# Optimization experiments

Hardware: AMD Instinct MI355X
Metric: run time of the kernel (lower is better)

## Reference

```python
import math
import jax, jax.numpy as jnp
import numpy as np

NUM_TOKENS = 8192
MODEL_DIM = 1024
NUM_EXPERTS = 64
CAPACITY_FACTOR = 1.0
MIN_CAPACITY = 8
SHIFT_PRIORITY = 0.5
LOAD_BALANCE_W = 0.01


def setup_inputs() -> dict:
    key = jax.random.key(0)
    k1, k2 = jax.random.split(key)
    x = jax.random.normal(k1, (NUM_TOKENS, MODEL_DIM), dtype=jnp.float32)
    # torch.nn.Linear(model_dim, num_experts, bias=False).weight -> [E, D]
    wg_weight = jax.random.normal(k2, (NUM_EXPERTS, MODEL_DIM), dtype=jnp.float32) * 0.02
    return {"x": x, "wg_weight": wg_weight}


def reference(x, wg_weight):
    S = x.shape[0]
    E = wg_weight.shape[0]
    # gate projection (fp32, as in DeepSpeed gating)
    logits = jnp.einsum('sd,ed->se', x, wg_weight)  # [S, E]
    gates = jax.nn.softmax(logits, axis=1)
    original_gates = gates

    # _capacity: ceil(S/E * capacity_factor), clamped to min_capacity (static)
    capacity = max(int(math.ceil(S / E * CAPACITY_FACTOR)), MIN_CAPACITY)

    indices1_s = jnp.argmax(gates, axis=1)                      # [S]
    mask1 = jax.nn.one_hot(indices1_s, E, dtype=jnp.int32)      # [S, E]
    exp_counts = jnp.sum(mask1, axis=0)                         # [E]

    # AuxLoss: GShard load-balance loss, zloss/entropy weights are 0
    me = jnp.mean(gates, axis=0)
    ce = jnp.mean(mask1.astype(gates.dtype), axis=0)
    l_aux = jnp.sum(me * ce) * E * LOAD_BALANCE_W

    # shifted-priority routing: sort tokens by -max_gate, roll, positional cumsum
    importance_scores = -jnp.max(gates, axis=1)                 # [S]
    sort_indices = jnp.argsort(importance_scores)               # [S]
    shift_num = int(S * SHIFT_PRIORITY)                         # static
    sort_indices = jnp.roll(sort_indices, shift_num)
    recover_indices = jnp.argsort(sort_indices)
    sorted_mask1 = mask1[sort_indices]                          # [S, E]
    sorted_cumsum1 = (jnp.cumsum(sorted_mask1, axis=0) - 1) * sorted_mask1
    locations1 = sorted_cumsum1[recover_indices]                # [S, E]

    # capacity dropping
    mask1 = mask1 * (locations1 < capacity).astype(jnp.int32)
    locations1_s = jnp.sum(locations1 * mask1, axis=1)          # [S]

    gates_masked = original_gates * mask1.astype(gates.dtype)   # [S, E]
    locations1_sc = jax.nn.one_hot(locations1_s, capacity, dtype=gates.dtype)  # [S, C]
    combine_weights = jnp.einsum('se,sc->sec', gates_masked, locations1_sc)    # [S, E, C]
    dispatch_mask = combine_weights.astype(bool)

    unrouted_token_rate = 1.0 - jnp.mean(jnp.any(dispatch_mask, axis=(-1, -2)).astype(jnp.float32))
    return l_aux, combine_weights, dispatch_mask, exp_counts, unrouted_token_rate
```

## Files before the change

### kernel.cpp

```cpp
#include <hip/hip_runtime.h>
#include <stdint.h>

#define S_TOK   8192
#define MODEL_D 1024
#define N_EXP   64
#define CAP     128
#define SHIFT   4096
#define SLAB    (N_EXP * CAP)
#define CDSIZE  ((size_t)S_TOK * SLAB)


#define OFF_EXPERT   0
#define OFF_GATE     32768
#define OFF_KEY      65536
#define OFF_KEY2     98304
#define OFF_LOC      131072
#define OFF_MEPART   163840
#define OFF_HIST     229376
#define OFF_DROP     294912
#define OFF_WGT      295936

__device__ __forceinline__ unsigned f2key(float f) {
    unsigned b = __float_as_uint(f);
    return (b & 0x80000000u) ? ~b : (b | 0x80000000u);
}

__global__ __launch_bounds__(256) void k0_transpose(const float* __restrict__ wg,
                                                    float* __restrict__ wgT) {
    int id0 = blockIdx.x * 256 + threadIdx.x;
#pragma unroll
    for (int i = 0; i < 4; ++i) {
        int id = id0 + i * 16384;
        int e = id >> 10;
        int d = id & 1023;
        wgT[d * 64 + e] = wg[id];
    }
}

__global__ __launch_bounds__(256) void k1_gemm_softmax(
    const float* __restrict__ x, const float* __restrict__ wgT,
    int* __restrict__ expert_id, float* __restrict__ gate1,
    unsigned* __restrict__ keys, float* __restrict__ me_part,
    int* __restrict__ hist_part)
{
    __shared__ float lg[32][65];
    __shared__ float mrow[32], zrow[32];
    __shared__ int   exrow[32];
    __shared__ int   hist[64];
    __shared__ float mep[4][64];

    const int tid  = threadIdx.x;
    const int lane = tid & 63;
    const int wave = __builtin_amdgcn_readfirstlane(tid >> 6);
    const int tokBase = blockIdx.x * 32 + wave * 8;

    float acc[8] = {0.f,0.f,0.f,0.f,0.f,0.f,0.f,0.f};
    const float* xrow = x + (size_t)tokBase * MODEL_D;

    for (int d = 0; d < MODEL_D; d += 4) {
        float w0 = wgT[(d + 0) * 64 + lane];
        float w1 = wgT[(d + 1) * 64 + lane];
        float w2 = wgT[(d + 2) * 64 + lane];
        float w3 = wgT[(d + 3) * 64 + lane];
#pragma unroll
        for (int t = 0; t < 8; ++t) {
            const float* xr = xrow + t * MODEL_D + d;
            acc[t] = fmaf(xr[0], w0, acc[t]);
            acc[t] = fmaf(xr[1], w1, acc[t]);
            acc[t] = fmaf(xr[2], w2, acc[t]);
            acc[t] = fmaf(xr[3], w3, acc[t]);
        }
    }
#pragma unroll
    for (int t = 0; t < 8; ++t) lg[wave * 8 + t][lane] = acc[t];
    __syncthreads();

    if (tid < 64) hist[tid] = 0;
    if (tid < 32) {
        const int t = tid;
        float m = lg[t][0]; int am = 0;
        for (int e = 1; e < 64; ++e) {
            float v = lg[t][e];
            if (v > m) { m = v; am = e; }
        }
        float z = 0.f;
        for (int e = 0; e < 64; ++e) z += expf(lg[t][e] - m);
        float rz = 1.0f / z;
        mrow[t] = m; zrow[t] = rz; exrow[t] = am;
        int sG = blockIdx.x * 32 + t;
        expert_id[sG] = am;
        gate1[sG] = rz;
        keys[sG] = f2key(-rz);
    }
    __syncthreads();

    if (tid < 32) atomicAdd(&hist[exrow[tid]], 1);
    {
        const int e = tid & 63, tg = tid >> 6;
        float p = 0.f;
        for (int t = tg; t < 32; t += 4) p += expf(lg[t][e] - mrow[t]) * zrow[t];
        mep[tg][e] = p;
    }
    __syncthreads();

    if (tid < 64) {
        me_part[blockIdx.x * 64 + tid] = mep[0][tid] + mep[1][tid] + mep[2][tid] + mep[3][tid];
        hist_part[blockIdx.x * 64 + tid] = hist[tid];
    }
}

__global__ __launch_bounds__(256) void k2_rank(const unsigned* __restrict__ keys,
                                               const int* __restrict__ expert_id,
                                               unsigned* __restrict__ key2)
{
    __shared__ uint4 k4[2048];
    const int tid = threadIdx.x;
    const uint4* kg = (const uint4*)keys;
    for (int i = tid; i < 2048; i += 256) k4[i] = kg[i];
    __syncthreads();

    const int sl = tid >> 3, part = tid & 7;
    const int sG = blockIdx.x * 32 + sl;
    const unsigned myk = ((const unsigned*)k4)[sG];
    int cnt = 0;
    const int qbase = part * 256;
    for (int q = 0; q < 256; ++q) {
        uint4 v = k4[qbase + q];
        int j = (qbase + q) * 4;
        cnt += (v.x < myk) || (v.x == myk && (j + 0) < sG);
        cnt += (v.y < myk) || (v.y == myk && (j + 1) < sG);
        cnt += (v.z < myk) || (v.z == myk && (j + 2) < sG);
        cnt += (v.w < myk) || (v.w == myk && (j + 3) < sG);
    }
    cnt += __shfl_down(cnt, 4);
    cnt += __shfl_down(cnt, 2);
    cnt += __shfl_down(cnt, 1);
    if (part == 0) {
        int pos = (cnt + SHIFT) & (S_TOK - 1);
        key2[sG] = ((unsigned)expert_id[sG] << 13) | (unsigned)pos;
    }
}

__global__ __launch_bounds__(256) void k3_loc(const unsigned* __restrict__ key2,
                                              int* __restrict__ loc,
                                              int* __restrict__ drop_part)
{
    __shared__ uint4 k4[2048];
    __shared__ int dropc;
    const int tid = threadIdx.x;
    if (tid == 0) dropc = 0;
    const uint4* kg = (const uint4*)key2;
    for (int i = tid; i < 2048; i += 256) k4[i] = kg[i];
    __syncthreads();

    const int sl = tid >> 3, part = tid & 7;
    const int sG = blockIdx.x * 32 + sl;
    const unsigned myk = ((const unsigned*)k4)[sG];
    const unsigned lo = myk & ~8191u;
    int cnt = 0;
    const int qbase = part * 256;
    for (int q = 0; q < 256; ++q) {
        uint4 v = k4[qbase + q];
        cnt += (v.x >= lo) && (v.x < myk);
        cnt += (v.y >= lo) && (v.y < myk);
        cnt += (v.z >= lo) && (v.z < myk);
        cnt += (v.w >= lo) && (v.w < myk);
    }
    cnt += __shfl_down(cnt, 4);
    cnt += __shfl_down(cnt, 2);
    cnt += __shfl_down(cnt, 1);
    if (part == 0) {
        loc[sG] = cnt;
        if (cnt >= CAP) atomicAdd(&dropc, 1);
    }
    __syncthreads();
    if (tid == 0) drop_part[blockIdx.x] = dropc;
}

__global__ __launch_bounds__(256) void k4_write(const int* __restrict__ expert_id,
                                                const float* __restrict__ gate1,
                                                const int* __restrict__ loc,
                                                const float* __restrict__ me_part,
                                                const int* __restrict__ hist_part,
                                                const int* __restrict__ drop_part,
                                                float* __restrict__ out)
{
    const int b = blockIdx.x;
    if (b < S_TOK) {
        const int es = expert_id[b];
        const int lc = loc[b];
        const float g = gate1[b];
        const bool kept = (lc < CAP);
        const int hot = es * CAP + lc;
        float* outC = out + 1 + (size_t)b * SLAB;
        float* outD = outC + CDSIZE;
        for (int i = threadIdx.x; i < SLAB; i += 256) {
            bool is = kept && (i == hot);
            outC[i] = is ? g : 0.0f;
            outD[i] = is ? 1.0f : 0.0f;
        }
    } else {
        __shared__ float contrib[64];
        const int tid = threadIdx.x;
        if (tid < 64) {
            float ms = 0.f; int hs = 0;
            for (int p = 0; p < 256; ++p) {
                ms += me_part[p * 64 + tid];
                hs += hist_part[p * 64 + tid];
            }
            out[1 + 2 * CDSIZE + tid] = (float)hs;
            contrib[tid] = (ms * (1.0f / S_TOK)) * ((float)hs * (1.0f / S_TOK));
        }
        __syncthreads();
        if (tid == 0) {
            float sum = 0.f;
            for (int e = 0; e < 64; ++e) sum += contrib[e];
            out[0] = sum * (float)N_EXP * 0.01f;
            int dr = 0;
            for (int p = 0; p < 256; ++p) dr += drop_part[p];
            out[1 + 2 * CDSIZE + 64] = (float)dr * (1.0f / S_TOK);
        }
    }
}

extern "C" void kernel_launch(void* const* d_in, const int* in_sizes, int n_in,
                              void* d_out, int out_size, void* d_ws, size_t ws_size,
                              hipStream_t stream) {
    (void)in_sizes; (void)n_in; (void)out_size; (void)ws_size;
    const float* x  = (const float*)d_in[0];
    const float* wg = (const float*)d_in[1];
    float* out = (float*)d_out;
    char* ws = (char*)d_ws;

    int*      expert_id = (int*)(ws + OFF_EXPERT);
    float*    gate1     = (float*)(ws + OFF_GATE);
    unsigned* keys      = (unsigned*)(ws + OFF_KEY);
    unsigned* key2      = (unsigned*)(ws + OFF_KEY2);
    int*      loc       = (int*)(ws + OFF_LOC);
    float*    me_part   = (float*)(ws + OFF_MEPART);
    int*      hist_part = (int*)(ws + OFF_HIST);
    int*      drop_part = (int*)(ws + OFF_DROP);
    float*    wgT       = (float*)(ws + OFF_WGT);

    hipLaunchKernelGGL(k0_transpose,    dim3(64),   dim3(256), 0, stream, wg, wgT);
    hipLaunchKernelGGL(k1_gemm_softmax, dim3(256),  dim3(256), 0, stream, x, wgT,
                       expert_id, gate1, keys, me_part, hist_part);
    hipLaunchKernelGGL(k2_rank,         dim3(256),  dim3(256), 0, stream, keys, expert_id, key2);
    hipLaunchKernelGGL(k3_loc,          dim3(256),  dim3(256), 0, stream, key2, loc, drop_part);
    hipLaunchKernelGGL(k4_write,        dim3(8193), dim3(256), 0, stream,
                       expert_id, gate1, loc, me_part, hist_part, drop_part, out);
}
```

Measured before the change: 753.2 us.

## Zero-fill output with vector stores and scatter hot entries; stage x in LDS

The per-token slab writer is replaced by a grid-stride float4 zero fill of the whole output. The location kernel then scatters only the single nonzero combine and dispatch entry per kept token, and the load-balance reduction moves into a small one-block final kernel. The gate GEMM now stages x chunks in shared memory and reads a float4-repacked weight layout. The rank loops rotate their start index per part, which is meant to reduce LDS bank conflicts. The cost is an extra ordering dependency: the fill must finish before the scatter writes.

```diff
diff --git a/kernel.cpp b/kernel.cpp
--- a/kernel.cpp
+++ b/kernel.cpp
@@ -8,13 +8,13 @@
 #define SHIFT   4096
 #define SLAB    (N_EXP * CAP)
 #define CDSIZE  ((size_t)S_TOK * SLAB)
+#define OUT_FILL4 33554448
 
 
 #define OFF_EXPERT   0
 #define OFF_GATE     32768
 #define OFF_KEY      65536
 #define OFF_KEY2     98304
-#define OFF_LOC      131072
 #define OFF_MEPART   163840
 #define OFF_HIST     229376
 #define OFF_DROP     294912
@@ -25,24 +25,32 @@
     return (b & 0x80000000u) ? ~b : (b | 0x80000000u);
 }
 
-__global__ __launch_bounds__(256) void k0_transpose(const float* __restrict__ wg,
-                                                    float* __restrict__ wgT) {
+__global__ __launch_bounds__(256) void k_fill(float4* __restrict__ out4) {
+    const float4 z = make_float4(0.f, 0.f, 0.f, 0.f);
+    size_t i = (size_t)blockIdx.x * 256 + threadIdx.x;
+    const size_t stride = (size_t)gridDim.x * 256;
+    for (; i < OUT_FILL4; i += stride) out4[i] = z;
+}
+
+__global__ __launch_bounds__(256) void k0_repack(const float* __restrict__ wg,
+                                                 float* __restrict__ wgT4) {
     int id0 = blockIdx.x * 256 + threadIdx.x;
 #pragma unroll
     for (int i = 0; i < 4; ++i) {
         int id = id0 + i * 16384;
         int e = id >> 10;
         int d = id & 1023;
-        wgT[d * 64 + e] = wg[id];
+        wgT4[((d >> 2) * 64 + e) * 4 + (d & 3)] = wg[id];
     }
 }
 
 __global__ __launch_bounds__(256) void k1_gemm_softmax(
-    const float* __restrict__ x, const float* __restrict__ wgT,
+    const float* __restrict__ x, const float* __restrict__ wgT4,
     int* __restrict__ expert_id, float* __restrict__ gate1,
     unsigned* __restrict__ keys, float* __restrict__ me_part,
     int* __restrict__ hist_part)
 {
+    __shared__ float xs[32][256];
     __shared__ float lg[32][65];
     __shared__ float mrow[32], zrow[32];
     __shared__ int   exrow[32];
@@ -51,28 +59,41 @@
 
     const int tid  = threadIdx.x;
     const int lane = tid & 63;
-    const int wave = __builtin_amdgcn_readfirstlane(tid >> 6);
-    const int tokBase = blockIdx.x * 32 + wave * 8;
+    const int wv   = tid >> 6;
+    const int tok0 = blockIdx.x * 32;
+
+    const float4* xg  = (const float4*)x;
+    const float4* wg4 = (const float4*)wgT4;
 
     float acc[8] = {0.f,0.f,0.f,0.f,0.f,0.f,0.f,0.f};
-    const float* xrow = x + (size_t)tokBase * MODEL_D;
-
-    for (int d = 0; d < MODEL_D; d += 4) {
-        float w0 = wgT[(d + 0) * 64 + lane];
-        float w1 = wgT[(d + 1) * 64 + lane];
-        float w2 = wgT[(d + 2) * 64 + lane];
-        float w3 = wgT[(d + 3) * 64 + lane];
-#pragma unroll
-        for (int t = 0; t < 8; ++t) {
-            const float* xr = xrow + t * MODEL_D + d;
-            acc[t] = fmaf(xr[0], w0, acc[t]);
-            acc[t] = fmaf(xr[1], w1, acc[t]);
-            acc[t] = fmaf(xr[2], w2, acc[t]);
-            acc[t] = fmaf(xr[3], w3, acc[t]);
-        }
-    }
-#pragma unroll
-    for (int t = 0; t < 8; ++t) lg[wave * 8 + t][lane] = acc[t];
+
+    for (int chunk = 0; chunk < 4; ++chunk) {
+        __syncthreads();
+#pragma unroll
+        for (int i = 0; i < 8; ++i) {
+            int linear = tid + 256 * i;
+            int t  = linear >> 6;
+            int c4 = linear & 63;
+            ((float4*)xs)[t * 64 + c4] = xg[(size_t)(tok0 + t) * 256 + chunk * 64 + c4];
+        }
+        __syncthreads();
+
+#pragma unroll 4
+        for (int dd = 0; dd < 256; dd += 4) {
+            int d = chunk * 256 + dd;
+            float4 w = wg4[(d >> 2) * 64 + lane];
+#pragma unroll
+            for (int t = 0; t < 8; ++t) {
+                float4 xv = *(const float4*)&xs[wv * 8 + t][dd];
+                acc[t] = fmaf(xv.x, w.x, acc[t]);
+                acc[t] = fmaf(xv.y, w.y, acc[t]);
+                acc[t] = fmaf(xv.z, w.z, acc[t]);
+                acc[t] = fmaf(xv.w, w.w, acc[t]);
+            }
+        }
+    }
+#pragma unroll
+    for (int t = 0; t < 8; ++t) lg[wv * 8 + t][lane] = acc[t];
     __syncthreads();
 
     if (tid < 64) hist[tid] = 0;
@@ -87,7 +108,7 @@
         for (int e = 0; e < 64; ++e) z += expf(lg[t][e] - m);
         float rz = 1.0f / z;
         mrow[t] = m; zrow[t] = rz; exrow[t] = am;
-        int sG = blockIdx.x * 32 + t;
+        int sG = tok0 + t;
         expert_id[sG] = am;
         gate1[sG] = rz;
         keys[sG] = f2key(-rz);
@@ -125,8 +146,9 @@
     int cnt = 0;
     const int qbase = part * 256;
     for (int q = 0; q < 256; ++q) {
-        uint4 v = k4[qbase + q];
-        int j = (qbase + q) * 4;
+        int qq = (q + part) & 255;
+        uint4 v = k4[qbase + qq];
+        int j = (qbase + qq) * 4;
         cnt += (v.x < myk) || (v.x == myk && (j + 0) < sG);
         cnt += (v.y < myk) || (v.y == myk && (j + 1) < sG);
         cnt += (v.z < myk) || (v.z == myk && (j + 2) < sG);
@@ -141,9 +163,10 @@
     }
 }
 
-__global__ __launch_bounds__(256) void k3_loc(const unsigned* __restrict__ key2,
-                                              int* __restrict__ loc,
-                                              int* __restrict__ drop_part)
+__global__ __launch_bounds__(256) void k3_loc_scatter(const unsigned* __restrict__ key2,
+                                                      const float* __restrict__ gate1,
+                                                      float* __restrict__ out,
+                                                      int* __restrict__ drop_part)
 {
     __shared__ uint4 k4[2048];
     __shared__ int dropc;
@@ -160,7 +183,8 @@
     int cnt = 0;
     const int qbase = part * 256;
     for (int q = 0; q < 256; ++q) {
-        uint4 v = k4[qbase + q];
+        int qq = (q + part) & 255;
+        uint4 v = k4[qbase + qq];
         cnt += (v.x >= lo) && (v.x < myk);
         cnt += (v.y >= lo) && (v.y < myk);
         cnt += (v.z >= lo) && (v.z < myk);
@@ -170,56 +194,50 @@
     cnt += __shfl_down(cnt, 2);
     cnt += __shfl_down(cnt, 1);
     if (part == 0) {
-        loc[sG] = cnt;
-        if (cnt >= CAP) atomicAdd(&dropc, 1);
+        if (cnt >= CAP) {
+            atomicAdd(&dropc, 1);
+        } else {
+            unsigned e = myk >> 13;
+            size_t idx = 1 + (size_t)sG * SLAB + (size_t)e * CAP + (unsigned)cnt;
+            out[idx] = gate1[sG];
+            out[idx + CDSIZE] = 1.0f;
+        }
     }
     __syncthreads();
     if (tid == 0) drop_part[blockIdx.x] = dropc;
 }
 
-__global__ __launch_bounds__(256) void k4_write(const int* __restrict__ expert_id,
-                                                const float* __restrict__ gate1,
-                                                const int* __restrict__ loc,
-                                                const float* __restrict__ me_part,
-                                                const int* __restrict__ hist_part,
-                                                const int* __restrict__ drop_part,
-                                                float* __restrict__ out)
-{
-    const int b = blockIdx.x;
-    if (b < S_TOK) {
-        const int es = expert_id[b];
-        const int lc = loc[b];
-        const float g = gate1[b];
-        const bool kept = (lc < CAP);
-        const int hot = es * CAP + lc;
-        float* outC = out + 1 + (size_t)b * SLAB;
-        float* outD = outC + CDSIZE;
-        for (int i = threadIdx.x; i < SLAB; i += 256) {
-            bool is = kept && (i == hot);
-            outC[i] = is ? g : 0.0f;
-            outD[i] = is ? 1.0f : 0.0f;
-        }
-    } else {
-        __shared__ float contrib[64];
-        const int tid = threadIdx.x;
-        if (tid < 64) {
-            float ms = 0.f; int hs = 0;
-            for (int p = 0; p < 256; ++p) {
-                ms += me_part[p * 64 + tid];
-                hs += hist_part[p * 64 + tid];
-            }
-            out[1 + 2 * CDSIZE + tid] = (float)hs;
-            contrib[tid] = (ms * (1.0f / S_TOK)) * ((float)hs * (1.0f / S_TOK));
-        }
-        __syncthreads();
-        if (tid == 0) {
-            float sum = 0.f;
-            for (int e = 0; e < 64; ++e) sum += contrib[e];
-            out[0] = sum * (float)N_EXP * 0.01f;
-            int dr = 0;
-            for (int p = 0; p < 256; ++p) dr += drop_part[p];
-            out[1 + 2 * CDSIZE + 64] = (float)dr * (1.0f / S_TOK);
-        }
+__global__ __launch_bounds__(256) void k_final(const float* __restrict__ me_part,
+                                               const int* __restrict__ hist_part,
+                                               const int* __restrict__ drop_part,
+                                               float* __restrict__ out)
+{
+    __shared__ float msum[4][64];
+    __shared__ int   hsum[4][64];
+    __shared__ float contrib[64];
+    const int tid = threadIdx.x;
+    const int e = tid & 63, qt = tid >> 6;
+    float ms = 0.f; int hs = 0;
+    for (int p = qt * 64; p < qt * 64 + 64; ++p) {
+        ms += me_part[p * 64 + e];
+        hs += hist_part[p * 64 + e];
+    }
+    msum[qt][e] = ms; hsum[qt][e] = hs;
+    __syncthreads();
+    if (tid < 64) {
+        float m = msum[0][tid] + msum[1][tid] + msum[2][tid] + msum[3][tid];
+        int   h = hsum[0][tid] + hsum[1][tid] + hsum[2][tid] + hsum[3][tid];
+        out[1 + 2 * CDSIZE + tid] = (float)h;
+        contrib[tid] = (m * (1.0f / S_TOK)) * ((float)h * (1.0f / S_TOK));
+    }
+    __syncthreads();
+    if (tid == 0) {
+        float sum = 0.f;
+        for (int i = 0; i < 64; ++i) sum += contrib[i];
+        out[0] = sum * (float)N_EXP * 0.01f;
+        int dr = 0;
+        for (int p = 0; p < 256; ++p) dr += drop_part[p];
+        out[1 + 2 * CDSIZE + 64] = (float)dr * (1.0f / S_TOK);
     }
 }
 
@@ -236,17 +254,17 @@
     float*    gate1     = (float*)(ws + OFF_GATE);
     unsigned* keys      = (unsigned*)(ws + OFF_KEY);
     unsigned* key2      = (unsigned*)(ws + OFF_KEY2);
-    int*      loc       = (int*)(ws + OFF_LOC);
     float*    me_part   = (float*)(ws + OFF_MEPART);
     int*      hist_part = (int*)(ws + OFF_HIST);
     int*      drop_part = (int*)(ws + OFF_DROP);
-    float*    wgT       = (float*)(ws + OFF_WGT);
-
-    hipLaunchKernelGGL(k0_transpose,    dim3(64),   dim3(256), 0, stream, wg, wgT);
-    hipLaunchKernelGGL(k1_gemm_softmax, dim3(256),  dim3(256), 0, stream, x, wgT,
+    float*    wgT4      = (float*)(ws + OFF_WGT);
+
+    hipLaunchKernelGGL(k_fill,          dim3(8192), dim3(256), 0, stream, (float4*)out);
+    hipLaunchKernelGGL(k0_repack,       dim3(64),   dim3(256), 0, stream, wg, wgT4);
+    hipLaunchKernelGGL(k1_gemm_softmax, dim3(256),  dim3(256), 0, stream, x, wgT4,
                        expert_id, gate1, keys, me_part, hist_part);
     hipLaunchKernelGGL(k2_rank,         dim3(256),  dim3(256), 0, stream, keys, expert_id, key2);
-    hipLaunchKernelGGL(k3_loc,          dim3(256),  dim3(256), 0, stream, key2, loc, drop_part);
-    hipLaunchKernelGGL(k4_write,        dim3(8193), dim3(256), 0, stream,
-                       expert_id, gate1, loc, me_part, hist_part, drop_part, out);
-}
+    hipLaunchKernelGGL(k3_loc_scatter,  dim3(256),  dim3(256), 0, stream, key2, gate1, out, drop_part);
+    hipLaunchKernelGGL(k_final,         dim3(1),    dim3(256), 0, stream,
+                       me_part, hist_part, drop_part, out);
+}
```

New measurement: 796.5 us. 5.7% more time.
